# Kernel optimization log

Hardware: AMD Instinct MI355X
Metric: run time of the kernel (lower is better)

## Reference

```python
import jax, jax.numpy as jnp
import numpy as np

N = 4096
F_IN = 512
ALPHA = 0.2          # LeakyReLU negative slope
NEG_INF = -9e15      # mask fill used by pyGAT


def setup_inputs() -> dict:
    key = jax.random.key(0)
    ks = jax.random.split(key, 9)
    x = jax.random.normal(ks[0], (N, F_IN), dtype=jnp.float32)
    adj = (jax.random.uniform(ks[1], (N, N)) < 0.005).astype(jnp.float32)
    adj = jnp.maximum(adj, jnp.eye(N, dtype=jnp.float32))
    s = 0.05
    W1 = jax.random.normal(ks[2], (512, 8, 128), dtype=jnp.float32) * s
    a_src1 = jax.random.normal(ks[3], (8, 128), dtype=jnp.float32) * s
    a_dst1 = jax.random.normal(ks[4], (8, 128), dtype=jnp.float32) * s
    W2 = jax.random.normal(ks[5], (1024, 1, 16), dtype=jnp.float32) * s
    a_src2 = jax.random.normal(ks[6], (1, 16), dtype=jnp.float32) * s
    a_dst2 = jax.random.normal(ks[7], (1, 16), dtype=jnp.float32) * s
    return {"x": x, "adj": adj, "W1": W1, "a_src1": a_src1, "a_dst1": a_dst1,
            "W2": W2, "a_src2": a_src2, "a_dst2": a_dst2}


def gat_layer(x, mask, W, a_src, a_dst, concat, activation):
    # x: [N, Fin], W: [Fin, H, Fout]
    h = jnp.einsum('nf,fho->nho', x, W)                  # [N, H, Fout]
    f_src = jnp.einsum('nho,ho->hn', h, a_src)            # [H, N]
    f_dst = jnp.einsum('nho,ho->hn', h, a_dst)            # [H, N]
    e = f_src[:, :, None] + f_dst[:, None, :]             # [H, N, N]
    e = jax.nn.leaky_relu(e, ALPHA)
    e = jnp.where(mask[None, :, :], e, NEG_INF)
    attn = jax.nn.softmax(e, axis=-1)                     # masked softmax over neighbors j
    out = jnp.einsum('hij,jho->iho', attn, h)             # [N, H, Fout]
    if concat:
        out = out.reshape(out.shape[0], -1)               # [N, H*Fout]
    else:
        out = out.mean(axis=1)                            # [N, Fout]
    if activation:
        out = jax.nn.elu(out)
    return out


def reference(x, adj, W1, a_src1, a_dst1, W2, a_src2, a_dst2):
    mask = adj > 0
    h1 = gat_layer(x, mask, W1, a_src1, a_dst1, concat=True, activation=True)
    h2 = gat_layer(h1, mask, W2, a_src2, a_dst2, concat=False, activation=False)
    out = jax.nn.elu(h2)
    return jax.nn.log_softmax(out, axis=1)
```

## Files before the change

### kernel.cpp

```cpp
#include <hip/hip_runtime.h>
#include <hip/hip_bf16.h>
#include <hip/hip_fp16.h>

typedef __attribute__((ext_vector_type(8))) short short8;
typedef __attribute__((ext_vector_type(8))) _Float16 half8;
typedef __attribute__((ext_vector_type(2))) _Float16 h2v;
typedef __attribute__((ext_vector_type(4))) float f32x4;

#define MAXNBR 128
#define ALPHA 0.2f

static __device__ __forceinline__ unsigned short f2h(float f) {
    return __half_as_ushort(__float2half(f));
}
static __device__ __forceinline__ float h2f(unsigned short u) {
    return __half2float(__ushort_as_half(u));
}

__global__ __launch_bounds__(256) void cvt(const float* __restrict__ x,
                                           unsigned short* __restrict__ xh,
                                           const float* __restrict__ W1,
                                           unsigned short* __restrict__ W1t) {
    int b = blockIdx.x, t = threadIdx.x;
    if (b < 1024) {
        size_t base = (size_t)b * 2048 + t * 8;
        float4 v0 = *(const float4*)&x[base];
        float4 v1 = *(const float4*)&x[base + 4];
        short8 o;
        o[0] = f2h(v0.x); o[1] = f2h(v0.y); o[2] = f2h(v0.z); o[3] = f2h(v0.w);
        o[4] = f2h(v1.x); o[5] = f2h(v1.y); o[6] = f2h(v1.z); o[7] = f2h(v1.w);
        *(short8*)&xh[base] = o;
    } else {
        int idx = (b - 1024) * 256 + t;
        int c = idx >> 9, k = idx & 511;
        W1t[idx] = f2h(W1[(size_t)k * 1024 + c]);
    }
}

__global__ __launch_bounds__(256) void gemm_scan(const unsigned short* __restrict__ A,
                                                 const unsigned short* __restrict__ Bt,
                                                 unsigned short* __restrict__ C,
                                                 const float* __restrict__ adj,
                                                 int* __restrict__ nbr_idx,
                                                 int* __restrict__ nbr_cnt) {
    __shared__ unsigned short Asm[128 * 64];
    __shared__ unsigned short Bsm[64 * 64];
    int b = blockIdx.x;
    int tid = threadIdx.x;
    if (b < 512) {
        int lane = tid & 63;
        int w = tid >> 6;
        int wr = w >> 1, wc = w & 1;
        int rowBase = (b & 31) * 128, colBase = (b >> 5) * 64;
        int lr = lane >> 3;
        int lc = (lane & 7) * 8;
        f32x4 acc[4][2] = {};
        for (int k0 = 0; k0 < 512; k0 += 64) {
            #pragma unroll
            for (int i = 0; i < 4; ++i) {
                int rA = i * 32 + w * 8;
                __builtin_amdgcn_global_load_lds(
                    (const __attribute__((address_space(1))) void*)&A[(size_t)(rowBase + rA + lr) * 512 + k0 + lc],
                    (__attribute__((address_space(3))) void*)&Asm[rA * 64],
                    16, 0, 0);
            }
            #pragma unroll
            for (int i = 0; i < 2; ++i) {
                int rB = i * 32 + w * 8;
                __builtin_amdgcn_global_load_lds(
                    (const __attribute__((address_space(1))) void*)&Bt[(size_t)(colBase + rB + lr) * 512 + k0 + lc],
                    (__attribute__((address_space(3))) void*)&Bsm[rB * 64],
                    16, 0, 0);
            }
            __syncthreads();
            #pragma unroll
            for (int kk = 0; kk < 64; kk += 32) {
                half8 af[4], bfv[2];
                int kf = kk + (lane >> 4) * 8;
                #pragma unroll
                for (int m = 0; m < 4; ++m)
                    af[m] = *(const half8*)&Asm[(wr * 64 + m * 16 + (lane & 15)) * 64 + kf];
                #pragma unroll
                for (int n = 0; n < 2; ++n)
                    bfv[n] = *(const half8*)&Bsm[(wc * 32 + n * 16 + (lane & 15)) * 64 + kf];
                #pragma unroll
                for (int m = 0; m < 4; ++m)
                    #pragma unroll
                    for (int n = 0; n < 2; ++n)
                        acc[m][n] = __builtin_amdgcn_mfma_f32_16x16x32_f16(af[m], bfv[n], acc[m][n], 0, 0, 0);
            }
            __syncthreads();
        }
        int crow0 = rowBase + wr * 64, ccol0 = colBase + wc * 32;
        #pragma unroll
        for (int m = 0; m < 4; ++m)
            #pragma unroll
            for (int n = 0; n < 2; ++n) {
                int col = ccol0 + n * 16 + (lane & 15);
                int row0 = crow0 + m * 16 + (lane >> 4) * 4;
                #pragma unroll
                for (int r = 0; r < 4; ++r)
                    C[(size_t)(row0 + r) * 1024 + col] = f2h(acc[m][n][r]);
            }
    } else {
        int row = (b - 512) * 4 + (tid >> 6);
        int lane = tid & 63;
        const float* arow = adj + (size_t)row * 4096;
        int cnt = 0;
        for (int base = 0; base < 4096; base += 256) {
            float4 v = *(const float4*)&arow[base + lane * 4];
            #pragma unroll
            for (int s = 0; s < 4; ++s) {
                float xv = ((const float*)&v)[s];
                unsigned long long m = __ballot(xv > 0.f);
                if (xv > 0.f) {
                    int pos = cnt + (int)__popcll(m & ((1ull << lane) - 1ull));
                    if (pos < MAXNBR) nbr_idx[row * MAXNBR + pos] = base + lane * 4 + s;
                }
                cnt += (int)__popcll(m);
            }
        }
        if (lane == 0) nbr_cnt[row] = cnt < MAXNBR ? cnt : MAXNBR;
    }
}

__global__ __launch_bounds__(256) void attn_coef1(const unsigned short* __restrict__ h1h,
                                                  const float* __restrict__ a_src,
                                                  const float* __restrict__ a_dst,
                                                  float* __restrict__ fsp,
                                                  float* __restrict__ fdp) {
    int n = blockIdx.x, t = threadIdx.x;
    ushort4 v = *(const ushort4*)&h1h[(size_t)n * 1024 + t * 4];
    int head = t >> 5;
    int o0 = (t * 4) & 127;
    float hv0 = h2f(v.x), hv1 = h2f(v.y), hv2 = h2f(v.z), hv3 = h2f(v.w);
    float ps = hv0 * a_src[head * 128 + o0] + hv1 * a_src[head * 128 + o0 + 1]
             + hv2 * a_src[head * 128 + o0 + 2] + hv3 * a_src[head * 128 + o0 + 3];
    float pd = hv0 * a_dst[head * 128 + o0] + hv1 * a_dst[head * 128 + o0 + 1]
             + hv2 * a_dst[head * 128 + o0 + 2] + hv3 * a_dst[head * 128 + o0 + 3];
    #pragma unroll
    for (int off = 1; off < 32; off <<= 1) {
        ps += __shfl_xor(ps, off);
        pd += __shfl_xor(pd, off);
    }
    if ((t & 31) == 0) {
        fsp[n * 8 + head] = ps;
        fdp[n * 8 + head] = pd;
    }
}

__global__ __launch_bounds__(256, 8) void aggregate5(const unsigned short* __restrict__ h1h,
                                                     const int* __restrict__ nbr_idx,
                                                     const int* __restrict__ nbr_cnt,
                                                     const float* __restrict__ fsp,
                                                     const float* __restrict__ fdp,
                                                     unsigned short* __restrict__ h1act) {
    __shared__ int nbr[MAXNBR];
    __shared__ float e_s[8][MAXNBR];
    __shared__ _Float16 attwS[8][MAXNBR];
    __shared__ half8 partS[128];
    int i = blockIdx.x;
    int t = threadIdx.x;
    int cnt = nbr_cnt[i];
    if (t < MAXNBR) nbr[t] = (t < cnt) ? nbr_idx[i * MAXNBR + t] : 0;
    __syncthreads();
    if (t < MAXNBR) {
        if (t < cnt) {
            int nb = nbr[t];
            float4 fs0 = *(const float4*)&fsp[i * 8];
            float4 fs1 = *(const float4*)&fsp[i * 8 + 4];
            float4 d0 = *(const float4*)&fdp[nb * 8];
            float4 d1 = *(const float4*)&fdp[nb * 8 + 4];
            float e0 = fs0.x + d0.x, e1 = fs0.y + d0.y, e2 = fs0.z + d0.z, e3 = fs0.w + d0.w;
            float e4 = fs1.x + d1.x, e5 = fs1.y + d1.y, e6 = fs1.z + d1.z, e7 = fs1.w + d1.w;
            e_s[0][t] = e0 > 0.f ? e0 : ALPHA * e0;
            e_s[1][t] = e1 > 0.f ? e1 : ALPHA * e1;
            e_s[2][t] = e2 > 0.f ? e2 : ALPHA * e2;
            e_s[3][t] = e3 > 0.f ? e3 : ALPHA * e3;
            e_s[4][t] = e4 > 0.f ? e4 : ALPHA * e4;
            e_s[5][t] = e5 > 0.f ? e5 : ALPHA * e5;
            e_s[6][t] = e6 > 0.f ? e6 : ALPHA * e6;
            e_s[7][t] = e7 > 0.f ? e7 : ALPHA * e7;
        } else {
            #pragma unroll
            for (int h = 0; h < 8; ++h) e_s[h][t] = -INFINITY;
        }
    }
    __syncthreads();
    {
        int h = t >> 5, sl = t & 31;
        float e[4];
        #pragma unroll
        for (int p = 0; p < 4; ++p) e[p] = e_s[h][sl + p * 32];
        float m = fmaxf(fmaxf(e[0], e[1]), fmaxf(e[2], e[3]));
        #pragma unroll
        for (int off = 1; off < 32; off <<= 1) m = fmaxf(m, __shfl_xor(m, off));
        float wq[4], s = 0.f;
        #pragma unroll
        for (int p = 0; p < 4; ++p) {
            wq[p] = (e[p] == -INFINITY) ? 0.f : __expf(e[p] - m);
            s += wq[p];
        }
        #pragma unroll
        for (int off = 1; off < 32; off <<= 1) s += __shfl_xor(s, off);
        float inv = 1.f / s;
        #pragma unroll
        for (int p = 0; p < 4; ++p)
            attwS[h][sl + p * 32] = (_Float16)(wq[p] * inv);
    }
    __syncthreads();
    int tf = t & 127;
    int par = t >> 7;
    int head = tf >> 4;
    const unsigned short* src = h1h + tf * 8;
    h2v acc2[4] = {};
    int cntPad = (cnt + 3) & ~3;
    for (int j = par; j < cntPad; j += 4) {
        int nb1 = nbr[j], nb2 = nbr[j + 2];
        _Float16 w1 = attwS[head][j], w2 = attwS[head][j + 2];
        half8 v1 = *(const half8*)&src[(size_t)nb1 << 10];
        half8 v2 = *(const half8*)&src[(size_t)nb2 << 10];
        h2v w1v = (h2v){w1, w1}, w2v = (h2v){w2, w2};
        const h2v* p1 = (const h2v*)&v1;
        const h2v* p2 = (const h2v*)&v2;
        #pragma unroll
        for (int q = 0; q < 4; ++q)
            acc2[q] += w1v * p1[q] + w2v * p2[q];
    }
    if (par == 1) {
        half8 st;
        #pragma unroll
        for (int q = 0; q < 4; ++q) { st[q * 2] = acc2[q][0]; st[q * 2 + 1] = acc2[q][1]; }
        partS[tf] = st;
    }
    __syncthreads();
    if (par == 0) {
        half8 p = partS[tf];
        short8 o;
        #pragma unroll
        for (int q = 0; q < 4; ++q) {
            float a0 = (float)acc2[q][0] + (float)p[q * 2];
            float a1 = (float)acc2[q][1] + (float)p[q * 2 + 1];
            a0 = a0 > 0.f ? a0 : (__expf(a0) - 1.f);
            a1 = a1 > 0.f ? a1 : (__expf(a1) - 1.f);
            o[q * 2] = f2h(a0);
            o[q * 2 + 1] = f2h(a1);
        }
        *(short8*)&h1act[(size_t)i * 1024 + tf * 8] = o;
    }
}

__global__ __launch_bounds__(256) void layer2_mfma(const unsigned short* __restrict__ h1act,
                                                   const float* __restrict__ W2,
                                                   const float* __restrict__ a_src2,
                                                   const float* __restrict__ a_dst2,
                                                   float* __restrict__ h2,
                                                   float2* __restrict__ fsd2) {
    __shared__ unsigned short Asm2[64 * 64];
    __shared__ unsigned short W2t[16 * 1032];
    int t = threadIdx.x, lane = t & 63, w = t >> 6;
    int rowBase = blockIdx.x * 64;
    for (int idx = t; idx < 16384; idx += 256) {
        int k = idx >> 4, o = idx & 15;
        W2t[o * 1032 + k] = f2h(W2[idx]);
    }
    f32x4 acc = {};
    __syncthreads();
    for (int k0 = 0; k0 < 1024; k0 += 64) {
        #pragma unroll
        for (int r = 0; r < 2; ++r) {
            int rA = r * 32 + w * 8;
            __builtin_amdgcn_global_load_lds(
                (const __attribute__((address_space(1))) void*)&h1act[(size_t)(rowBase + rA + (lane >> 3)) * 1024 + k0 + (lane & 7) * 8],
                (__attribute__((address_space(3))) void*)&Asm2[rA * 64],
                16, 0, 0);
        }
        __syncthreads();
        #pragma unroll
        for (int kk = 0; kk < 64; kk += 32) {
            half8 af = *(const half8*)&Asm2[(w * 16 + (lane & 15)) * 64 + kk + (lane >> 4) * 8];
            half8 bf = *(const half8*)&W2t[(lane & 15) * 1032 + k0 + kk + (lane >> 4) * 8];
            acc = __builtin_amdgcn_mfma_f32_16x16x32_f16(af, bf, acc, 0, 0, 0);
        }
        __syncthreads();
    }
    int col = lane & 15;
    int g = lane >> 4;
    #pragma unroll
    for (int r = 0; r < 4; ++r) {
        int row = rowBase + w * 16 + g * 4 + r;
        float v = acc[r];
        h2[row * 16 + col] = v;
        float ps = v * a_src2[col];
        float pd = v * a_dst2[col];
        #pragma unroll
        for (int off = 1; off < 16; off <<= 1) {
            ps += __shfl_xor(ps, off);
            pd += __shfl_xor(pd, off);
        }
        if (col == 0) fsd2[row] = make_float2(ps, pd);
    }
}

__global__ __launch_bounds__(64) void final_layer(const float* __restrict__ h2,
                                                  const int* __restrict__ nbr_idx,
                                                  const int* __restrict__ nbr_cnt,
                                                  const float2* __restrict__ fsd2,
                                                  float* __restrict__ out) {
    __shared__ float attn[MAXNBR];
    __shared__ int nbr[MAXNBR];
    int i = blockIdx.x;
    int l = threadIdx.x;
    int cnt = nbr_cnt[i];
    float fsi = fsd2[i].x;
    for (int j = l; j < MAXNBR; j += 64) {
        float e = -INFINITY;
        if (j < cnt) {
            int jj = nbr_idx[i * MAXNBR + j];
            nbr[j] = jj;
            float xv = fsi + fsd2[jj].y;
            e = xv > 0.f ? xv : ALPHA * xv;
        }
        attn[j] = e;
    }
    __syncthreads();
    float m = fmaxf(attn[l], attn[l + 64]);
    #pragma unroll
    for (int off = 1; off < 64; off <<= 1) m = fmaxf(m, __shfl_xor(m, off));
    float s = 0.f;
    {
        float e0 = attn[l], e1 = attn[l + 64];
        if (e0 != -INFINITY) s += __expf(e0 - m);
        if (e1 != -INFINITY) s += __expf(e1 - m);
    }
    #pragma unroll
    for (int off = 1; off < 64; off <<= 1) s += __shfl_xor(s, off);
    for (int j = l; j < MAXNBR; j += 64) {
        float e = attn[j];
        attn[j] = (e == -INFINITY) ? 0.f : __expf(e - m) / s;
    }
    __syncthreads();
    if (l < 16) {
        float acc = 0.f;
        for (int j = 0; j < cnt; ++j)
            acc += attn[j] * h2[nbr[j] * 16 + l];
        float v = acc > 0.f ? acc : expm1f(acc);
        float mx = v;
        #pragma unroll
        for (int off = 1; off < 16; off <<= 1) mx = fmaxf(mx, __shfl_xor(mx, off));
        float se = __expf(v - mx);
        #pragma unroll
        for (int off = 1; off < 16; off <<= 1) se += __shfl_xor(se, off);
        out[i * 16 + l] = v - mx - logf(se);
    }
}

extern "C" void kernel_launch(void* const* d_in, const int* in_sizes, int n_in,
                              void* d_out, int out_size, void* d_ws, size_t ws_size,
                              hipStream_t stream) {
    const float* x      = (const float*)d_in[0];
    const float* adj    = (const float*)d_in[1];
    const float* W1     = (const float*)d_in[2];
    const float* a_src1 = (const float*)d_in[3];
    const float* a_dst1 = (const float*)d_in[4];
    const float* W2     = (const float*)d_in[5];
    const float* a_src2 = (const float*)d_in[6];
    const float* a_dst2 = (const float*)d_in[7];
    float* out = (float*)d_out;

    char* ws = (char*)d_ws;
    unsigned short* xh    = (unsigned short*)ws;
    unsigned short* w1t   = (unsigned short*)(ws + (4u << 20));
    unsigned short* h1h   = (unsigned short*)(ws + (6u << 20));
    float* fsp   = (float*)(ws + (14u << 20));
    float* fdp   = (float*)(ws + (14u << 20) + (128u << 10));
    float* h2    = (float*)(ws + (15u << 20));
    float2* fsd2 = (float2*)(ws + (15u << 20) + (256u << 10));
    int* nbr_idx = (int*)(ws + (16u << 20));
    int* nbr_cnt = (int*)(ws + (18u << 20));
    unsigned short* h1act = (unsigned short*)(ws + (26u << 20));

    cvt<<<3072, 256, 0, stream>>>(x, xh, W1, w1t);
    gemm_scan<<<1536, 256, 0, stream>>>(xh, w1t, h1h, adj, nbr_idx, nbr_cnt);
    attn_coef1<<<4096, 256, 0, stream>>>(h1h, a_src1, a_dst1, fsp, fdp);
    aggregate5<<<4096, 256, 0, stream>>>(h1h, nbr_idx, nbr_cnt, fsp, fdp, h1act);
    layer2_mfma<<<64, 256, 0, stream>>>(h1act, W2, a_src2, a_dst2, h2, fsd2);
    final_layer<<<4096, 64, 0, stream>>>(h2, nbr_idx, nbr_cnt, fsd2, out);
}
```

Before: 72.95 us.

## Fuse attention coefficients into GEMM epilogue, widen aggregate, split-K layer-2 GEMM

Computes the per-head source/destination attention dot products inside the layer-1 GEMM epilogue, accumulating with atomics into a pre-zeroed buffer, which removes the separate attn_coef1 kernel and its reread of h1. The aggregation kernel moves to 512 threads with four-way neighbour partitioning and a three-way partial reduction. The layer-2 GEMM uses 256 blocks of 16 rows with split-K across waves, reducing through shared memory, to give more parallelism than 64 blocks. In exchange it adds a memset, atomics whose summation order is non-deterministic, and higher register and LDS use in the aggregate kernel.

```diff
diff --git a/kernel.cpp b/kernel.cpp
--- a/kernel.cpp
+++ b/kernel.cpp
@@ -42,7 +42,11 @@
                                                  unsigned short* __restrict__ C,
                                                  const float* __restrict__ adj,
                                                  int* __restrict__ nbr_idx,
-                                                 int* __restrict__ nbr_cnt) {
+                                                 int* __restrict__ nbr_cnt,
+                                                 const float* __restrict__ a_src1,
+                                                 const float* __restrict__ a_dst1,
+                                                 float* __restrict__ fsp,
+                                                 float* __restrict__ fdp) {
     __shared__ unsigned short Asm[128 * 64];
     __shared__ unsigned short Bsm[64 * 64];
     int b = blockIdx.x;
@@ -102,6 +106,30 @@
                 for (int r = 0; r < 4; ++r)
                     C[(size_t)(row0 + r) * 1024 + col] = f2h(acc[m][n][r]);
             }
+        {
+            int head = colBase >> 7;
+            float as0 = a_src1[ccol0 + (lane & 15)];
+            float as1v = a_src1[ccol0 + 16 + (lane & 15)];
+            float ad0 = a_dst1[ccol0 + (lane & 15)];
+            float ad1v = a_dst1[ccol0 + 16 + (lane & 15)];
+            #pragma unroll
+            for (int m = 0; m < 4; ++m)
+                #pragma unroll
+                for (int r = 0; r < 4; ++r) {
+                    float ps = acc[m][0][r] * as0 + acc[m][1][r] * as1v;
+                    float pd = acc[m][0][r] * ad0 + acc[m][1][r] * ad1v;
+                    #pragma unroll
+                    for (int off = 1; off < 16; off <<= 1) {
+                        ps += __shfl_xor(ps, off);
+                        pd += __shfl_xor(pd, off);
+                    }
+                    if ((lane & 15) == 0) {
+                        int row = crow0 + m * 16 + (lane >> 4) * 4 + r;
+                        atomicAdd(&fsp[row * 8 + head], ps);
+                        atomicAdd(&fdp[row * 8 + head], pd);
+                    }
+                }
+        }
     } else {
         int row = (b - 512) * 4 + (tid >> 6);
         int lane = tid & 63;
@@ -124,41 +152,16 @@
     }
 }
 
-__global__ __launch_bounds__(256) void attn_coef1(const unsigned short* __restrict__ h1h,
-                                                  const float* __restrict__ a_src,
-                                                  const float* __restrict__ a_dst,
-                                                  float* __restrict__ fsp,
-                                                  float* __restrict__ fdp) {
-    int n = blockIdx.x, t = threadIdx.x;
-    ushort4 v = *(const ushort4*)&h1h[(size_t)n * 1024 + t * 4];
-    int head = t >> 5;
-    int o0 = (t * 4) & 127;
-    float hv0 = h2f(v.x), hv1 = h2f(v.y), hv2 = h2f(v.z), hv3 = h2f(v.w);
-    float ps = hv0 * a_src[head * 128 + o0] + hv1 * a_src[head * 128 + o0 + 1]
-             + hv2 * a_src[head * 128 + o0 + 2] + hv3 * a_src[head * 128 + o0 + 3];
-    float pd = hv0 * a_dst[head * 128 + o0] + hv1 * a_dst[head * 128 + o0 + 1]
-             + hv2 * a_dst[head * 128 + o0 + 2] + hv3 * a_dst[head * 128 + o0 + 3];
-    #pragma unroll
-    for (int off = 1; off < 32; off <<= 1) {
-        ps += __shfl_xor(ps, off);
-        pd += __shfl_xor(pd, off);
-    }
-    if ((t & 31) == 0) {
-        fsp[n * 8 + head] = ps;
-        fdp[n * 8 + head] = pd;
-    }
-}
-
-__global__ __launch_bounds__(256, 8) void aggregate5(const unsigned short* __restrict__ h1h,
-                                                     const int* __restrict__ nbr_idx,
-                                                     const int* __restrict__ nbr_cnt,
-                                                     const float* __restrict__ fsp,
-                                                     const float* __restrict__ fdp,
-                                                     unsigned short* __restrict__ h1act) {
+__global__ __launch_bounds__(512) void aggregate6(const unsigned short* __restrict__ h1h,
+                                                  const int* __restrict__ nbr_idx,
+                                                  const int* __restrict__ nbr_cnt,
+                                                  const float* __restrict__ fsp,
+                                                  const float* __restrict__ fdp,
+                                                  unsigned short* __restrict__ h1act) {
     __shared__ int nbr[MAXNBR];
     __shared__ float e_s[8][MAXNBR];
     __shared__ _Float16 attwS[8][MAXNBR];
-    __shared__ half8 partS[128];
+    __shared__ half8 partS[3][128];
     int i = blockIdx.x;
     int t = threadIdx.x;
     int cnt = nbr_cnt[i];
@@ -187,7 +190,7 @@
         }
     }
     __syncthreads();
-    {
+    if (t < 256) {
         int h = t >> 5, sl = t & 31;
         float e[4];
         #pragma unroll
@@ -216,31 +219,29 @@
     h2v acc2[4] = {};
     int cntPad = (cnt + 3) & ~3;
     for (int j = par; j < cntPad; j += 4) {
-        int nb1 = nbr[j], nb2 = nbr[j + 2];
-        _Float16 w1 = attwS[head][j], w2 = attwS[head][j + 2];
-        half8 v1 = *(const half8*)&src[(size_t)nb1 << 10];
-        half8 v2 = *(const half8*)&src[(size_t)nb2 << 10];
-        h2v w1v = (h2v){w1, w1}, w2v = (h2v){w2, w2};
-        const h2v* p1 = (const h2v*)&v1;
-        const h2v* p2 = (const h2v*)&v2;
+        int nb = nbr[j];
+        _Float16 wv = attwS[head][j];
+        half8 v = *(const half8*)&src[(size_t)nb << 10];
+        h2v wvv = (h2v){wv, wv};
+        const h2v* pv = (const h2v*)&v;
         #pragma unroll
         for (int q = 0; q < 4; ++q)
-            acc2[q] += w1v * p1[q] + w2v * p2[q];
-    }
-    if (par == 1) {
+            acc2[q] += wvv * pv[q];
+    }
+    if (par > 0) {
         half8 st;
         #pragma unroll
         for (int q = 0; q < 4; ++q) { st[q * 2] = acc2[q][0]; st[q * 2 + 1] = acc2[q][1]; }
-        partS[tf] = st;
+        partS[par - 1][tf] = st;
     }
     __syncthreads();
     if (par == 0) {
-        half8 p = partS[tf];
+        half8 p0 = partS[0][tf], p1 = partS[1][tf], p2 = partS[2][tf];
         short8 o;
         #pragma unroll
         for (int q = 0; q < 4; ++q) {
-            float a0 = (float)acc2[q][0] + (float)p[q * 2];
-            float a1 = (float)acc2[q][1] + (float)p[q * 2 + 1];
+            float a0 = (float)acc2[q][0] + (float)p0[q * 2] + (float)p1[q * 2] + (float)p2[q * 2];
+            float a1 = (float)acc2[q][1] + (float)p0[q * 2 + 1] + (float)p1[q * 2 + 1] + (float)p2[q * 2 + 1];
             a0 = a0 > 0.f ? a0 : (__expf(a0) - 1.f);
             a1 = a1 > 0.f ? a1 : (__expf(a1) - 1.f);
             o[q * 2] = f2h(a0);
@@ -256,49 +257,40 @@
                                                    const float* __restrict__ a_dst2,
                                                    float* __restrict__ h2,
                                                    float2* __restrict__ fsd2) {
-    __shared__ unsigned short Asm2[64 * 64];
     __shared__ unsigned short W2t[16 * 1032];
+    __shared__ float pred[4][256];
     int t = threadIdx.x, lane = t & 63, w = t >> 6;
-    int rowBase = blockIdx.x * 64;
+    int rowBase = blockIdx.x * 16;
     for (int idx = t; idx < 16384; idx += 256) {
         int k = idx >> 4, o = idx & 15;
         W2t[o * 1032 + k] = f2h(W2[idx]);
     }
+    __syncthreads();
     f32x4 acc = {};
-    __syncthreads();
-    for (int k0 = 0; k0 < 1024; k0 += 64) {
-        #pragma unroll
-        for (int r = 0; r < 2; ++r) {
-            int rA = r * 32 + w * 8;
-            __builtin_amdgcn_global_load_lds(
-                (const __attribute__((address_space(1))) void*)&h1act[(size_t)(rowBase + rA + (lane >> 3)) * 1024 + k0 + (lane & 7) * 8],
-                (__attribute__((address_space(3))) void*)&Asm2[rA * 64],
-                16, 0, 0);
-        }
-        __syncthreads();
-        #pragma unroll
-        for (int kk = 0; kk < 64; kk += 32) {
-            half8 af = *(const half8*)&Asm2[(w * 16 + (lane & 15)) * 64 + kk + (lane >> 4) * 8];
-            half8 bf = *(const half8*)&W2t[(lane & 15) * 1032 + k0 + kk + (lane >> 4) * 8];
-            acc = __builtin_amdgcn_mfma_f32_16x16x32_f16(af, bf, acc, 0, 0, 0);
-        }
-        __syncthreads();
-    }
-    int col = lane & 15;
-    int g = lane >> 4;
+    int r0 = lane & 15, kg = (lane >> 4) * 8;
     #pragma unroll
-    for (int r = 0; r < 4; ++r) {
-        int row = rowBase + w * 16 + g * 4 + r;
-        float v = acc[r];
-        h2[row * 16 + col] = v;
-        float ps = v * a_src2[col];
-        float pd = v * a_dst2[col];
+    for (int kk = 0; kk < 256; kk += 32) {
+        int k0 = w * 256 + kk;
+        half8 af = *(const half8*)&h1act[(size_t)(rowBase + r0) * 1024 + k0 + kg];
+        half8 bf = *(const half8*)&W2t[r0 * 1032 + k0 + kg];
+        acc = __builtin_amdgcn_mfma_f32_16x16x32_f16(af, bf, acc, 0, 0, 0);
+    }
+    #pragma unroll
+    for (int r = 0; r < 4; ++r)
+        pred[w][((lane >> 4) * 4 + r) * 16 + (lane & 15)] = acc[r];
+    __syncthreads();
+    if (t < 256) {
+        int row = t >> 4, col = t & 15;
+        float s = pred[0][t] + pred[1][t] + pred[2][t] + pred[3][t];
+        h2[(rowBase + row) * 16 + col] = s;
+        float ps = s * a_src2[col];
+        float pd = s * a_dst2[col];
         #pragma unroll
         for (int off = 1; off < 16; off <<= 1) {
             ps += __shfl_xor(ps, off);
             pd += __shfl_xor(pd, off);
         }
-        if (col == 0) fsd2[row] = make_float2(ps, pd);
+        if (col == 0) fsd2[rowBase + row] = make_float2(ps, pd);
     }
 }
 
@@ -380,10 +372,11 @@
     int* nbr_cnt = (int*)(ws + (18u << 20));
     unsigned short* h1act = (unsigned short*)(ws + (26u << 20));
 
+    hipMemsetAsync(fsp, 0, 256u << 10, stream);
     cvt<<<3072, 256, 0, stream>>>(x, xh, W1, w1t);
-    gemm_scan<<<1536, 256, 0, stream>>>(xh, w1t, h1h, adj, nbr_idx, nbr_cnt);
-    attn_coef1<<<4096, 256, 0, stream>>>(h1h, a_src1, a_dst1, fsp, fdp);
-    aggregate5<<<4096, 256, 0, stream>>>(h1h, nbr_idx, nbr_cnt, fsp, fdp, h1act);
-    layer2_mfma<<<64, 256, 0, stream>>>(h1act, W2, a_src2, a_dst2, h2, fsd2);
+    gemm_scan<<<1536, 256, 0, stream>>>(xh, w1t, h1h, adj, nbr_idx, nbr_cnt,
+                                        a_src1, a_dst1, fsp, fdp);
+    aggregate6<<<4096, 512, 0, stream>>>(h1h, nbr_idx, nbr_cnt, fsp, fdp, h1act);
+    layer2_mfma<<<256, 256, 0, stream>>>(h1act, W2, a_src2, a_dst2, h2, fsd2);
     final_layer<<<4096, 64, 0, stream>>>(h2, nbr_idx, nbr_cnt, fsd2, out);
 }
```

Measured after the change: 86.25 us. 18.2% more time.
